# Kernel optimization log

Measured on AMD Instinct MI355X. Metric: run time of the kernel, lower is better.

Reference implementation:

```python
import jax, jax.numpy as jnp
import numpy as np

EPS = 1e-6

def _ln(x, g, b):
    mu = jnp.mean(x, axis=-1, keepdims=True)
    var = jnp.mean(jnp.square(x - mu), axis=-1, keepdims=True)
    return (x - mu) * jax.lax.rsqrt(var + EPS) * g + b

def setup_inputs() -> dict:
    key = jax.random.key(0)
    ks = jax.random.split(key, 8)
    B, T, D = 4, 4096, 1024
    H = 16
    Dff = 4 * D
    s = 1.0 / np.sqrt(D)
    sf = 1.0 / np.sqrt(Dff)
    return {
        "x": jax.random.normal(ks[0], (B, T, D), dtype=jnp.float32),
        "wq": jax.random.uniform(ks[1], (D, D), jnp.float32, -s, s),
        "wk": jax.random.uniform(ks[2], (D, D), jnp.float32, -s, s),
        "wv": jax.random.uniform(ks[3], (D, D), jnp.float32, -s, s),
        "wo": jax.random.uniform(ks[4], (D, D), jnp.float32, -s, s),
        "ln1_g": jnp.ones((D,), jnp.float32),
        "ln1_b": jnp.zeros((D,), jnp.float32),
        "w1": jax.random.uniform(ks[5], (D, Dff), jnp.float32, -s, s),
        "b1": jnp.zeros((Dff,), jnp.float32),
        "w2": jax.random.uniform(ks[6], (Dff, D), jnp.float32, -sf, sf),
        "b2": jnp.zeros((D,), jnp.float32),
        "ln2_g": jnp.ones((D,), jnp.float32),
        "ln2_b": jnp.zeros((D,), jnp.float32),
    }

def reference(x, wq, wk, wv, wo, ln1_g, ln1_b, w1, b1, w2, b2, ln2_g, ln2_b):
    B, T, D = x.shape
    H = 16
    dk = D // H
    x1 = _ln(x, ln1_g, ln1_b)
    q = (x1 @ wq).reshape(B, T, H, dk)
    k = (x1 @ wk).reshape(B, T, H, dk)
    v = (x1 @ wv).reshape(B, T, H, dk)
    # NOTE: faithful to source -- attention mixes HEADS at each token position
    # attn[b,t,h,g] = softmax_g( sum_d q[b,t,h,d]*k[b,t,g,d] / sqrt(dk) )
    attn = jax.nn.softmax(jnp.einsum('bthd,btgd->bthg', q / np.sqrt(dk), k), axis=-1)
    o = jnp.einsum('bthg,btgd->bthd', attn, v)
    # faithful head-major reshape: transpose(1,2).contiguous().view(B,T,-1)
    o = jnp.transpose(o, (0, 2, 1, 3)).reshape(B, T, H * dk)
    o = o @ wo
    q2 = _ln(o + x, ln1_g, ln1_b)  # same layer_norm params reused
    h = jax.nn.gelu(q2 @ w1 + b1, approximate=False)
    y = h @ w2 + b2 + q2
    return _ln(y, ln2_g, ln2_b)
```

## Files before the change

kernel.cpp:

```cpp
#include <hip/hip_runtime.h>


typedef __attribute__((ext_vector_type(8))) short s16x8;
typedef __attribute__((ext_vector_type(4))) short s16x4;
typedef __attribute__((ext_vector_type(4))) float f32x4;

__device__ __forceinline__ short f2bf(float x) {
  unsigned u = __builtin_bit_cast(unsigned, x);
  u = (u + 0x7FFFu + ((u >> 16) & 1u)) >> 16;
  return (short)u;
}
__device__ __forceinline__ float bf2f(short s) {
  unsigned u = ((unsigned)(unsigned short)s) << 16;
  return __builtin_bit_cast(float, u);
}

__device__ __forceinline__ void ld_g2l16(const short* g, const short* l) {
  __builtin_amdgcn_global_load_lds(
      (const __attribute__((address_space(1))) void*)g,
      (__attribute__((address_space(3))) void*)l, 16, 0, 0);
}

__device__ __forceinline__ s16x8 lds_read8(const short* smem, int off) {
  const __attribute__((address_space(3))) short* p =
      (const __attribute__((address_space(3))) short*)smem;
  return *(const __attribute__((address_space(3))) s16x8*)(p + off);
}

__device__ __forceinline__ float fast_gelu(float v) {
  float y = 0.7978845608f * (v + 0.044715f * v * v * v);
  float ay = fabsf(y);
  float t = __expf(-2.0f * ay);
  float th = (1.0f - t) * __frcp_rn(1.0f + t);
  th = (y >= 0.f) ? th : -th;
  return 0.5f * v * (1.0f + th);
}

#define MFMA16(va, vb, vc) \
  __builtin_amdgcn_mfma_f32_16x16x32_bf16(va, vb, vc, 0, 0, 0)

template <int EPI>
__global__ __launch_bounds__(512, 2) void gemm256(
    const short* __restrict__ A, const short* __restrict__ BT,
    void* __restrict__ outp, const float* __restrict__ bias, int N, int K) {
  extern __shared__ __align__(16) short smem[];

  const int t = threadIdx.x;
  const int lane = t & 63, w = t >> 6;
  const int wm = w >> 2, wn = w & 3;

  const int nbn = N >> 8;
  const int oi = (int)blockIdx.x;
  const int seq = oi >> 3;
  const int bq = seq / nbn;
  const int bm = (oi & 7) * 8 + bq;
  const int bn = seq - bq * nbn;

  const int l8 = lane >> 3;
  const int lcw = ((lane & 7) ^ l8) * 8;
  const short* gA = A + (size_t)(bm * 256 + w * 8 + l8) * K + lcw;
  const short* gB = BT + (size_t)(bn * 256 + w * 8 + l8) * K + lcw;
  const int lb = w * 512;

  auto stage = [&](const short* g, int bufo, int h, int kt) {
    const int go = h * 128 * K + kt * 64;
    ld_g2l16(g + go, smem + bufo + h * 8192 + lb);
    ld_g2l16(g + go + 64 * K, smem + bufo + h * 8192 + 4096 + lb);
  };

  const int fr = lane & 15, fc = lane >> 4;
  const int baseA = (wm * 128 + fr) * 64;
  const int baseB = (wn * 64 + fr) * 64;
  const int sl0 = (fc ^ (fr & 7)) * 8;
  const int sl1 = ((4 + fc) ^ (fr & 7)) * 8;

  f32x4 acc[8][4];
#pragma unroll
  for (int m = 0; m < 8; ++m)
#pragma unroll
    for (int n = 0; n < 4; ++n) acc[m][n] = (f32x4){0.f, 0.f, 0.f, 0.f};

  const int nt = K >> 6;

  stage(gA, 0, 0, 0);
  stage(gA, 0, 1, 0);
  stage(gB, 32768, 0, 0);
  stage(gB, 32768, 1, 0);
  if (nt > 1) {
    stage(gA, 16384, 0, 1);
    stage(gA, 16384, 1, 1);
    stage(gB, 49152, 0, 1);
    stage(gB, 49152, 1, 1);
    asm volatile("s_waitcnt vmcnt(8)" ::: "memory");
  } else {
    asm volatile("s_waitcnt vmcnt(0)" ::: "memory");
  }
  __builtin_amdgcn_s_barrier();
  asm volatile("" ::: "memory");

  for (int u = 0; u < nt; ++u) {
    const bool pf = (u + 2 < nt);
    const int pa = (u & 1) << 14;
    const int pb = 32768 + pa;

    s16x8 a0[4][2], a1[4][2], b0[2][2], b1[2][2];
#pragma unroll
    for (int mi = 0; mi < 4; ++mi) {
      a0[mi][0] = lds_read8(smem, pa + baseA + mi * 1024 + sl0);
      a0[mi][1] = lds_read8(smem, pa + baseA + mi * 1024 + sl1);
    }
#pragma unroll
    for (int ni = 0; ni < 2; ++ni) {
      b0[ni][0] = lds_read8(smem, pb + baseB + ni * 1024 + sl0);
      b0[ni][1] = lds_read8(smem, pb + baseB + ni * 1024 + sl1);
    }
#pragma unroll
    for (int ni = 0; ni < 2; ++ni) {
      b1[ni][0] = lds_read8(smem, pb + baseB + 2048 + ni * 1024 + sl0);
      b1[ni][1] = lds_read8(smem, pb + baseB + 2048 + ni * 1024 + sl1);
    }
#pragma unroll
    for (int mi = 0; mi < 4; ++mi) {
      a1[mi][0] = lds_read8(smem, pa + baseA + 4096 + mi * 1024 + sl0);
      a1[mi][1] = lds_read8(smem, pa + baseA + 4096 + mi * 1024 + sl1);
    }

    __builtin_amdgcn_s_setprio(1);
#pragma unroll
    for (int mi = 0; mi < 4; ++mi)
#pragma unroll
      for (int ni = 0; ni < 2; ++ni) {
        acc[mi][ni] = MFMA16(a0[mi][0], b0[ni][0], acc[mi][ni]);
        acc[mi][ni] = MFMA16(a0[mi][1], b0[ni][1], acc[mi][ni]);
      }
#pragma unroll
    for (int mi = 0; mi < 4; ++mi)
#pragma unroll
      for (int ni = 0; ni < 2; ++ni) {
        acc[mi][2 + ni] = MFMA16(a0[mi][0], b1[ni][0], acc[mi][2 + ni]);
        acc[mi][2 + ni] = MFMA16(a0[mi][1], b1[ni][1], acc[mi][2 + ni]);
      }
#pragma unroll
    for (int mi = 0; mi < 4; ++mi)
#pragma unroll
      for (int ni = 0; ni < 2; ++ni) {
        acc[4 + mi][2 + ni] = MFMA16(a1[mi][0], b1[ni][0], acc[4 + mi][2 + ni]);
        acc[4 + mi][2 + ni] = MFMA16(a1[mi][1], b1[ni][1], acc[4 + mi][2 + ni]);
      }
    __builtin_amdgcn_s_setprio(0);

    asm volatile("s_waitcnt lgkmcnt(0)" ::: "memory");
    __builtin_amdgcn_s_barrier();
    asm volatile("" ::: "memory");

    if (pf) {
      stage(gB, pb, 0, u + 2);
      stage(gB, pb, 1, u + 2);
      stage(gA, pa, 0, u + 2);
      stage(gA, pa, 1, u + 2);
    }

    __builtin_amdgcn_s_setprio(1);
#pragma unroll
    for (int mi = 0; mi < 4; ++mi)
#pragma unroll
      for (int ni = 0; ni < 2; ++ni) {
        acc[4 + mi][ni] = MFMA16(a1[mi][0], b0[ni][0], acc[4 + mi][ni]);
        acc[4 + mi][ni] = MFMA16(a1[mi][1], b0[ni][1], acc[4 + mi][ni]);
      }
    __builtin_amdgcn_s_setprio(0);

    if (pf) {
      asm volatile("s_waitcnt vmcnt(8)" ::: "memory");
    } else {
      asm volatile("s_waitcnt vmcnt(0)" ::: "memory");
    }
    __builtin_amdgcn_s_barrier();
    asm volatile("" ::: "memory");
  }

  const int mb = bm * 256 + wm * 128;
  const int nb = bn * 256 + wn * 64;
  const int cr = (lane >> 4) * 4;
  const int cc = lane & 15;
#pragma unroll
  for (int m = 0; m < 8; ++m) {
#pragma unroll
    for (int n = 0; n < 4; ++n) {
#pragma unroll
      for (int r = 0; r < 4; ++r) {
        const size_t row = (size_t)(mb + m * 16 + cr + r);
        const size_t col = (size_t)(nb + n * 16 + cc);
        float v = acc[m][n][r];
        if constexpr (EPI == 0) {
          ((short*)outp)[row * N + col] = f2bf(v);
        } else if constexpr (EPI == 1) {
          ((float*)outp)[row * N + col] = v;
        } else if constexpr (EPI == 2) {
          v += bias[col];
          ((short*)outp)[row * N + col] = f2bf(fast_gelu(v));
        } else {
          float prev = ((float*)outp)[row * N + col];
          v += prev;
          if (bias) v += bias[col];
          ((float*)outp)[row * N + col] = v;
        }
      }
    }
  }
}

template <int EPI>
__global__ __launch_bounds__(512, 4) void gemm128(
    const short* __restrict__ A, const short* __restrict__ BT,
    void* __restrict__ outp, const float* __restrict__ bias, int N, int K) {
  extern __shared__ __align__(16) short smem[];

  const int t = threadIdx.x;
  const int lane = t & 63, w = t >> 6;
  const int wm = w >> 2, wn = w & 3;

  const int nbn = N >> 8;
  const int oi = (int)blockIdx.x;
  const int seq = oi >> 3;
  const int bq = seq / nbn;
  const int bm = (oi & 7) * 16 + bq;
  const int bn = seq - bq * nbn;

  const int lr = lane >> 2;
  const int lc = ((lane & 3) - ((lane >> 3) & 3)) & 3;
  const short* gA = A + (size_t)(bm * 128 + lr) * K + lc * 8;
  const short* gB = BT + (size_t)(bn * 256 + lr) * K + lc * 8;

  auto stageT = [&](int par, int kt) {
    ld_g2l16(gA + (size_t)(w * 16) * K + kt * 32, smem + par + w * 512);
    ld_g2l16(gB + (size_t)(2 * w * 16) * K + kt * 32,
             smem + par + 4096 + 2 * w * 512);
    ld_g2l16(gB + (size_t)((2 * w + 1) * 16) * K + kt * 32,
             smem + par + 4096 + (2 * w + 1) * 512);
  };

  const int fr = lane & 15, fc = lane >> 4;
  const int sl = ((fc + (fr >> 1)) & 3) * 8;
  const int baseA = (wm * 64 + fr) * 32 + sl;
  const int baseB = 4096 + (wn * 64 + fr) * 32 + sl;

  f32x4 acc[4][4];
#pragma unroll
  for (int m = 0; m < 4; ++m)
#pragma unroll
    for (int n = 0; n < 4; ++n) acc[m][n] = (f32x4){0.f, 0.f, 0.f, 0.f};

  const int nt = K >> 5;

  stageT(0, 0);
  stageT(12288, 1);
  asm volatile("s_waitcnt vmcnt(3)" ::: "memory");
  __builtin_amdgcn_s_barrier();
  asm volatile("" ::: "memory");

  int pcur = 0, pnxt = 12288, pprv = 24576;
  for (int u = 0; u < nt; ++u) {
    const bool pf = (u + 2 < nt);

    if (pf) stageT(pprv, u + 2);

    s16x8 a[4], b[4];
#pragma unroll
    for (int i = 0; i < 4; ++i)
      a[i] = lds_read8(smem, pcur + baseA + i * 512);
#pragma unroll
    for (int i = 0; i < 4; ++i)
      b[i] = lds_read8(smem, pcur + baseB + i * 512);

    __builtin_amdgcn_s_setprio(1);
#pragma unroll
    for (int mi = 0; mi < 4; ++mi)
#pragma unroll
      for (int ni = 0; ni < 4; ++ni)
        acc[mi][ni] = MFMA16(a[mi], b[ni], acc[mi][ni]);
    __builtin_amdgcn_s_setprio(0);

    asm volatile("s_waitcnt lgkmcnt(0)" ::: "memory");
    if (pf) {
      asm volatile("s_waitcnt vmcnt(3)" ::: "memory");
    } else {
      asm volatile("s_waitcnt vmcnt(0)" ::: "memory");
    }
    __builtin_amdgcn_s_barrier();
    asm volatile("" ::: "memory");

    const int tmp = pcur;
    pcur = pnxt;
    pnxt = pprv;
    pprv = tmp;
  }

  const int mb = bm * 128 + wm * 64;
  const int nb = bn * 256 + wn * 64;
  const int cr = (lane >> 4) * 4;
  const int cc = lane & 15;
#pragma unroll
  for (int m = 0; m < 4; ++m) {
#pragma unroll
    for (int n = 0; n < 4; ++n) {
#pragma unroll
      for (int r = 0; r < 4; ++r) {
        const size_t row = (size_t)(mb + m * 16 + cr + r);
        const size_t col = (size_t)(nb + n * 16 + cc);
        float v = acc[m][n][r];
        if constexpr (EPI == 0) {
          ((short*)outp)[row * N + col] = f2bf(v);
        } else if constexpr (EPI == 1) {
          ((float*)outp)[row * N + col] = v;
        } else if constexpr (EPI == 2) {
          v += bias[col];
          ((short*)outp)[row * N + col] = f2bf(fast_gelu(v));
        } else {
          float prev = ((float*)outp)[row * N + col];
          v += prev;
          if (bias) v += bias[col];
          ((float*)outp)[row * N + col] = v;
        }
      }
    }
  }
}

__global__ __launch_bounds__(256) void ln_k(
    const float* __restrict__ in, const float* __restrict__ add,
    const float* __restrict__ g, const float* __restrict__ b,
    float* __restrict__ outf, short* __restrict__ outb) {
  const int row = blockIdx.x;
  const size_t off = (size_t)row * 1024;
  const int t = threadIdx.x;
  float4 v = ((const float4*)(in + off))[t];
  if (add) {
    float4 w = ((const float4*)(add + off))[t];
    v.x += w.x; v.y += w.y; v.z += w.z; v.w += w.w;
  }
  float s = v.x + v.y + v.z + v.w;
  float ss = v.x * v.x + v.y * v.y + v.z * v.z + v.w * v.w;
#pragma unroll
  for (int o = 32; o > 0; o >>= 1) {
    s += __shfl_xor(s, o, 64);
    ss += __shfl_xor(ss, o, 64);
  }
  __shared__ float ps[4], pss[4];
  const int lane = t & 63, wave = t >> 6;
  if (lane == 0) { ps[wave] = s; pss[wave] = ss; }
  __syncthreads();
  s = ps[0] + ps[1] + ps[2] + ps[3];
  ss = pss[0] + pss[1] + pss[2] + pss[3];
  const float mean = s * (1.0f / 1024.0f);
  const float var = ss * (1.0f / 1024.0f) - mean * mean;
  const float rstd = rsqrtf(var + 1e-6f);
  const float4 gv = ((const float4*)g)[t];
  const float4 bv = ((const float4*)b)[t];
  float4 o4;
  o4.x = (v.x - mean) * rstd * gv.x + bv.x;
  o4.y = (v.y - mean) * rstd * gv.y + bv.y;
  o4.z = (v.z - mean) * rstd * gv.z + bv.z;
  o4.w = (v.w - mean) * rstd * gv.w + bv.w;
  if (outf) ((float4*)(outf + off))[t] = o4;
  if (outb) {
    s16x4 ob;
    ob[0] = f2bf(o4.x); ob[1] = f2bf(o4.y);
    ob[2] = f2bf(o4.z); ob[3] = f2bf(o4.w);
    *(s16x4*)(outb + off + t * 4) = ob;
  }
}

__device__ __forceinline__ void wconv_tile(const float* __restrict__ W,
                                           short* __restrict__ WT, int K,
                                           int N, int n0, int k0,
                                           float (*tile)[33], int c, int r) {
#pragma unroll
  for (int rr = r; rr < 32; rr += 8)
    tile[rr][c] = W[(size_t)(k0 + rr) * N + n0 + c];
  __syncthreads();
#pragma unroll
  for (int rr = r; rr < 32; rr += 8)
    WT[(size_t)(n0 + rr) * K + k0 + c] = f2bf(tile[c][rr]);
}

__global__ __launch_bounds__(256) void wconv_all(
    const float* __restrict__ wq, const float* __restrict__ wk,
    const float* __restrict__ wv, const float* __restrict__ wo,
    const float* __restrict__ w1, const float* __restrict__ w2,
    short* __restrict__ WQKVT, short* __restrict__ WOT,
    short* __restrict__ W1T, short* __restrict__ W2aT,
    short* __restrict__ W2bT) {
  __shared__ float tile[32][33];
  const int t = threadIdx.x;
  const int c = t & 31, r = t >> 5;
  const int i = blockIdx.x;
  if (i < 4096) {
    const int seg = i >> 10, j = i & 1023;
    const int n0 = (j & 31) * 32, k0 = (j >> 5) * 32;
    const float* src = (seg == 0) ? wq : (seg == 1) ? wk : (seg == 2) ? wv : wo;
    short* dst = (seg == 3) ? WOT : WQKVT + (size_t)seg * 1024 * 1024;
    wconv_tile(src, dst, 1024, 1024, n0, k0, tile, c, r);
  } else if (i < 8192) {
    const int j = i - 4096;
    const int n0 = (j & 127) * 32, k0 = (j >> 7) * 32;
    wconv_tile(w1, W1T, 1024, 4096, n0, k0, tile, c, r);
  } else if (i < 10240) {
    const int j = i - 8192;
    const int n0 = (j & 31) * 32, k0 = (j >> 5) * 32;
    wconv_tile(w2, W2aT, 2048, 1024, n0, k0, tile, c, r);
  } else {
    const int j = i - 10240;
    const int n0 = (j & 31) * 32, k0 = (j >> 5) * 32;
    wconv_tile(w2 + (size_t)2048 * 1024, W2bT, 2048, 1024, n0, k0, tile, c, r);
  }
}

__global__ __launch_bounds__(256) void attn_k(const short* __restrict__ qkv,
                                              short* __restrict__ omix) {
  __shared__ float Qs[4][16][65];
  __shared__ float Ks[4][16][65];
  __shared__ float Vs[4][16][65];
  __shared__ float Ps[4][16][17];
  const int lane = threadIdx.x & 63;
  const int wave = threadIdx.x >> 6;
  const int tok = blockIdx.x * 4 + wave;
  const short* base = qkv + (size_t)tok * 3072;

#pragma unroll
  for (int half = 0; half < 2; half++) {
    const int e = half * 512 + lane * 8;
    const int h = e >> 6, d = e & 63;
    s16x8 rq = *(const s16x8*)(base + e);
    s16x8 rk = *(const s16x8*)(base + 1024 + e);
    s16x8 rv = *(const s16x8*)(base + 2048 + e);
#pragma unroll
    for (int j = 0; j < 8; j++) {
      Qs[wave][h][d + j] = bf2f(rq[j]);
      Ks[wave][h][d + j] = bf2f(rk[j]);
      Vs[wave][h][d + j] = bf2f(rv[j]);
    }
  }
  __syncthreads();

  const int h = lane & 15;
  const int g0 = (lane >> 4) * 4;
  float sc[4] = {0.f, 0.f, 0.f, 0.f};
  for (int d = 0; d < 64; d++) {
    const float qv = Qs[wave][h][d];
#pragma unroll
    for (int i = 0; i < 4; i++) sc[i] += qv * Ks[wave][g0 + i][d];
  }
#pragma unroll
  for (int i = 0; i < 4; i++) sc[i] *= 0.125f;
  float m = fmaxf(fmaxf(sc[0], sc[1]), fmaxf(sc[2], sc[3]));
  m = fmaxf(m, __shfl_xor(m, 16, 64));
  m = fmaxf(m, __shfl_xor(m, 32, 64));
  float e[4], sum = 0.f;
#pragma unroll
  for (int i = 0; i < 4; i++) { e[i] = __expf(sc[i] - m); sum += e[i]; }
  sum += __shfl_xor(sum, 16, 64);
  sum += __shfl_xor(sum, 32, 64);
  const float inv = __frcp_rn(sum);
#pragma unroll
  for (int i = 0; i < 4; i++) Ps[wave][h][g0 + i] = e[i] * inv;
  __syncthreads();

  const int d0 = (lane >> 4) * 16;
  float o[16];
#pragma unroll
  for (int dd = 0; dd < 16; dd++) o[dd] = 0.f;
  for (int gg = 0; gg < 16; gg++) {
    const float pv = Ps[wave][h][gg];
#pragma unroll
    for (int dd = 0; dd < 16; dd++) o[dd] += pv * Vs[wave][gg][d0 + dd];
  }

  const int b = tok >> 12, t = tok & 4095;
  const size_t dst =
      ((size_t)(b * 4096 + h * 256 + (t >> 4))) * 1024 + (t & 15) * 64 + d0;
  s16x8 w0, w1;
#pragma unroll
  for (int j = 0; j < 8; j++) { w0[j] = f2bf(o[j]); w1[j] = f2bf(o[8 + j]); }
  *(s16x8*)(omix + dst) = w0;
  *(s16x8*)(omix + dst + 8) = w1;
}

extern "C" void kernel_launch(void* const* d_in, const int* in_sizes, int n_in,
                              void* d_out, int out_size, void* d_ws,
                              size_t ws_size, hipStream_t stream) {
  const float* x    = (const float*)d_in[0];
  const float* wq   = (const float*)d_in[1];
  const float* wk   = (const float*)d_in[2];
  const float* wv   = (const float*)d_in[3];
  const float* wo   = (const float*)d_in[4];
  const float* ln1g = (const float*)d_in[5];
  const float* ln1b = (const float*)d_in[6];
  const float* w1   = (const float*)d_in[7];
  const float* b1   = (const float*)d_in[8];
  const float* w2   = (const float*)d_in[9];
  const float* b2   = (const float*)d_in[10];
  const float* ln2g = (const float*)d_in[11];
  const float* ln2b = (const float*)d_in[12];
  float* out = (float*)d_out;

  char* ws = (char*)d_ws;
  const size_t MB = 1024ull * 1024ull;
  const size_t NEEDED = 152 * MB;
  if (ws_size < NEEDED) return;

  short* QKV  = (short*)(ws + 0);
  short* Q2B  = (short*)(ws + 0);
  short* Hbuf = (short*)(ws + 32 * MB);
  short* X1 = (short*)(ws + 96 * MB);
  short* WQKVT = (short*)(ws + 128 * MB);
  short* WOT   = (short*)(ws + 134 * MB);
  short* W1T   = (short*)(ws + 136 * MB);
  short* W2aT  = (short*)(ws + 144 * MB);
  short* W2bT  = (short*)(ws + 148 * MB);

  const dim3 B256(256);
  const dim3 B512(512);
  const unsigned LDS256 = 131072;
  const unsigned LDS128 = 73728;

  static bool attr_done = false;
  if (!attr_done) {
    attr_done = true;
    void (*k0)(const short*, const short*, void*, const float*, int, int) =
        gemm256<0>;
    (void)hipFuncSetAttribute((const void*)k0,
        hipFuncAttributeMaxDynamicSharedMemorySize, (int)LDS256);
    void (*h1)(const short*, const short*, void*, const float*, int, int) =
        gemm128<1>;
    void (*h2)(const short*, const short*, void*, const float*, int, int) =
        gemm128<2>;
    void (*h4)(const short*, const short*, void*, const float*, int, int) =
        gemm128<4>;
    (void)hipFuncSetAttribute((const void*)h1,
        hipFuncAttributeMaxDynamicSharedMemorySize, (int)LDS128);
    (void)hipFuncSetAttribute((const void*)h2,
        hipFuncAttributeMaxDynamicSharedMemorySize, (int)LDS128);
    (void)hipFuncSetAttribute((const void*)h4,
        hipFuncAttributeMaxDynamicSharedMemorySize, (int)LDS128);
  }

  wconv_all<<<dim3(12288), B256, 0, stream>>>(wq, wk, wv, wo, w1, w2, WQKVT,
                                              WOT, W1T, W2aT, W2bT);

  ln_k<<<16384, B256, 0, stream>>>(x, nullptr, ln1g, ln1b, nullptr, X1);

  gemm256<0><<<dim3(768), B512, LDS256, stream>>>(X1, WQKVT, QKV, nullptr,
                                                  3072, 1024);

  attn_k<<<4096, B256, 0, stream>>>(QKV, X1);

  gemm128<1><<<dim3(512), B512, LDS128, stream>>>(X1, WOT, out, nullptr,
                                                  1024, 1024);

  ln_k<<<16384, B256, 0, stream>>>(out, x, ln1g, ln1b, out, Q2B);

  gemm128<2><<<dim3(1024), B512, LDS128, stream>>>(Q2B, W1T, Hbuf, b1,
                                                   2048, 1024);
  gemm128<4><<<dim3(512), B512, LDS128, stream>>>(Hbuf, W2aT, out, nullptr,
                                                  1024, 2048);

  gemm128<2><<<dim3(1024), B512, LDS128, stream>>>(Q2B, W1T + 2048 * 1024,
                                                   Hbuf, b1 + 2048, 2048,
                                                   1024);
  gemm128<4><<<dim3(512), B512, LDS128, stream>>>(Hbuf, W2bT, out, b2,
                                                  1024, 2048);

  ln_k<<<16384, B256, 0, stream>>>(out, nullptr, ln2g, ln2b, out, nullptr);
}
```

Before: 776.9 us.

## Restructure 256x256 GEMM into fine-grained staged pipeline and use it everywhere

Rewrites the 256x256 GEMM main loop to process two K-tiles per iteration, splitting each into four MFMA quadrants. Global-to-LDS loads for the next tile are issued in half-tile pieces between those quadrants, with a barrier between each piece. The 128-row GEMM variant is removed, and the output projection and both MLP GEMMs now launch the 256 tile kernel with half as many blocks. The aim is to overlap loads with MFMA work more evenly and to raise data reuse. The cost is many more barriers per iteration, and fewer blocks (256 or 512 on a large-CU device) may leave occupancy or wave balance worse.

```diff
diff --git a/kernel.cpp b/kernel.cpp
--- a/kernel.cpp
+++ b/kernel.cpp
@@ -39,6 +39,11 @@
 #define MFMA16(va, vb, vc) \
   __builtin_amdgcn_mfma_f32_16x16x32_bf16(va, vb, vc, 0, 0, 0)
 
+#define BARRIER() do { __builtin_amdgcn_s_barrier(); \
+                       asm volatile("" ::: "memory"); } while (0)
+#define LGKM0() asm volatile("s_waitcnt lgkmcnt(0)" ::: "memory")
+#define VMC(n) asm volatile("s_waitcnt vmcnt(" #n ")" ::: "memory")
+
 template <int EPI>
 __global__ __launch_bounds__(512, 2) void gemm256(
     const short* __restrict__ A, const short* __restrict__ BT,
@@ -62,7 +67,7 @@
   const short* gB = BT + (size_t)(bn * 256 + w * 8 + l8) * K + lcw;
   const int lb = w * 512;
 
-  auto stage = [&](const short* g, int bufo, int h, int kt) {
+  auto stageH = [&](const short* g, int bufo, int h, int kt) {
     const int go = h * 128 * K + kt * 64;
     ld_g2l16(g + go, smem + bufo + h * 8192 + lb);
     ld_g2l16(g + go + 64 * K, smem + bufo + h * 8192 + 4096 + lb);
@@ -80,51 +85,36 @@
 #pragma unroll
     for (int n = 0; n < 4; ++n) acc[m][n] = (f32x4){0.f, 0.f, 0.f, 0.f};
 
+  s16x8 a0[4][2], a1[4][2], b0[2][2], b1[2][2];
+
   const int nt = K >> 6;
 
-  stage(gA, 0, 0, 0);
-  stage(gA, 0, 1, 0);
-  stage(gB, 32768, 0, 0);
-  stage(gB, 32768, 1, 0);
-  if (nt > 1) {
-    stage(gA, 16384, 0, 1);
-    stage(gA, 16384, 1, 1);
-    stage(gB, 49152, 0, 1);
-    stage(gB, 49152, 1, 1);
-    asm volatile("s_waitcnt vmcnt(8)" ::: "memory");
-  } else {
-    asm volatile("s_waitcnt vmcnt(0)" ::: "memory");
-  }
-  __builtin_amdgcn_s_barrier();
-  asm volatile("" ::: "memory");
-
-  for (int u = 0; u < nt; ++u) {
-    const bool pf = (u + 2 < nt);
-    const int pa = (u & 1) << 14;
-    const int pb = 32768 + pa;
-
-    s16x8 a0[4][2], a1[4][2], b0[2][2], b1[2][2];
+  stageH(gA, 0, 0, 0);
+  stageH(gA, 0, 1, 0);
+  stageH(gB, 32768, 0, 0);
+  stageH(gB, 32768, 1, 0);
+  stageH(gA, 16384, 0, 1);
+  stageH(gA, 16384, 1, 1);
+  VMC(4);
+  BARRIER();
+
+  for (int it = 0; it < (nt >> 1); ++it) {
+    const int u = it << 1;
+    const bool more = (u + 2 < nt);
+
 #pragma unroll
     for (int mi = 0; mi < 4; ++mi) {
-      a0[mi][0] = lds_read8(smem, pa + baseA + mi * 1024 + sl0);
-      a0[mi][1] = lds_read8(smem, pa + baseA + mi * 1024 + sl1);
+      a0[mi][0] = lds_read8(smem, baseA + mi * 1024 + sl0);
+      a0[mi][1] = lds_read8(smem, baseA + mi * 1024 + sl1);
     }
 #pragma unroll
     for (int ni = 0; ni < 2; ++ni) {
-      b0[ni][0] = lds_read8(smem, pb + baseB + ni * 1024 + sl0);
-      b0[ni][1] = lds_read8(smem, pb + baseB + ni * 1024 + sl1);
-    }
-#pragma unroll
-    for (int ni = 0; ni < 2; ++ni) {
-      b1[ni][0] = lds_read8(smem, pb + baseB + 2048 + ni * 1024 + sl0);
-      b1[ni][1] = lds_read8(smem, pb + baseB + 2048 + ni * 1024 + sl1);
-    }
-#pragma unroll
-    for (int mi = 0; mi < 4; ++mi) {
-      a1[mi][0] = lds_read8(smem, pa + baseA + 4096 + mi * 1024 + sl0);
-      a1[mi][1] = lds_read8(smem, pa + baseA + 4096 + mi * 1024 + sl1);
-    }
-
+      b0[ni][0] = lds_read8(smem, 32768 + baseB + ni * 1024 + sl0);
+      b0[ni][1] = lds_read8(smem, 32768 + baseB + ni * 1024 + sl1);
+    }
+    stageH(gB, 49152, 0, u + 1);
+    BARRIER();
+    LGKM0();
     __builtin_amdgcn_s_setprio(1);
 #pragma unroll
     for (int mi = 0; mi < 4; ++mi)
@@ -133,6 +123,50 @@
         acc[mi][ni] = MFMA16(a0[mi][0], b0[ni][0], acc[mi][ni]);
         acc[mi][ni] = MFMA16(a0[mi][1], b0[ni][1], acc[mi][ni]);
       }
+    __builtin_amdgcn_s_setprio(0);
+    BARRIER();
+
+#pragma unroll
+    for (int mi = 0; mi < 4; ++mi) {
+      a1[mi][0] = lds_read8(smem, baseA + 4096 + mi * 1024 + sl0);
+      a1[mi][1] = lds_read8(smem, baseA + 4096 + mi * 1024 + sl1);
+    }
+    stageH(gB, 49152, 1, u + 1);
+    BARRIER();
+    LGKM0();
+    __builtin_amdgcn_s_setprio(1);
+#pragma unroll
+    for (int mi = 0; mi < 4; ++mi)
+#pragma unroll
+      for (int ni = 0; ni < 2; ++ni) {
+        acc[4 + mi][ni] = MFMA16(a1[mi][0], b0[ni][0], acc[4 + mi][ni]);
+        acc[4 + mi][ni] = MFMA16(a1[mi][1], b0[ni][1], acc[4 + mi][ni]);
+      }
+    __builtin_amdgcn_s_setprio(0);
+    BARRIER();
+
+#pragma unroll
+    for (int ni = 0; ni < 2; ++ni) {
+      b1[ni][0] = lds_read8(smem, 32768 + baseB + 2048 + ni * 1024 + sl0);
+      b1[ni][1] = lds_read8(smem, 32768 + baseB + 2048 + ni * 1024 + sl1);
+    }
+    if (more) stageH(gA, 0, 0, u + 2);
+    BARRIER();
+    LGKM0();
+    __builtin_amdgcn_s_setprio(1);
+#pragma unroll
+    for (int mi = 0; mi < 4; ++mi)
+#pragma unroll
+      for (int ni = 0; ni < 2; ++ni) {
+        acc[4 + mi][2 + ni] = MFMA16(a1[mi][0], b1[ni][0], acc[4 + mi][2 + ni]);
+        acc[4 + mi][2 + ni] = MFMA16(a1[mi][1], b1[ni][1], acc[4 + mi][2 + ni]);
+      }
+    __builtin_amdgcn_s_setprio(0);
+    BARRIER();
+
+    if (more) stageH(gA, 0, 1, u + 2);
+    BARRIER();
+    __builtin_amdgcn_s_setprio(1);
 #pragma unroll
     for (int mi = 0; mi < 4; ++mi)
 #pragma unroll
@@ -140,6 +174,66 @@
         acc[mi][2 + ni] = MFMA16(a0[mi][0], b1[ni][0], acc[mi][2 + ni]);
         acc[mi][2 + ni] = MFMA16(a0[mi][1], b1[ni][1], acc[mi][2 + ni]);
       }
+    __builtin_amdgcn_s_setprio(0);
+    if (more) {
+      VMC(4);
+    } else {
+      VMC(0);
+    }
+    BARRIER();
+
+#pragma unroll
+    for (int mi = 0; mi < 4; ++mi) {
+      a0[mi][0] = lds_read8(smem, 16384 + baseA + mi * 1024 + sl0);
+      a0[mi][1] = lds_read8(smem, 16384 + baseA + mi * 1024 + sl1);
+    }
+#pragma unroll
+    for (int ni = 0; ni < 2; ++ni) {
+      b0[ni][0] = lds_read8(smem, 49152 + baseB + ni * 1024 + sl0);
+      b0[ni][1] = lds_read8(smem, 49152 + baseB + ni * 1024 + sl1);
+    }
+    if (more) stageH(gB, 32768, 0, u + 2);
+    BARRIER();
+    LGKM0();
+    __builtin_amdgcn_s_setprio(1);
+#pragma unroll
+    for (int mi = 0; mi < 4; ++mi)
+#pragma unroll
+      for (int ni = 0; ni < 2; ++ni) {
+        acc[mi][ni] = MFMA16(a0[mi][0], b0[ni][0], acc[mi][ni]);
+        acc[mi][ni] = MFMA16(a0[mi][1], b0[ni][1], acc[mi][ni]);
+      }
+    __builtin_amdgcn_s_setprio(0);
+    BARRIER();
+
+#pragma unroll
+    for (int mi = 0; mi < 4; ++mi) {
+      a1[mi][0] = lds_read8(smem, 16384 + baseA + 4096 + mi * 1024 + sl0);
+      a1[mi][1] = lds_read8(smem, 16384 + baseA + 4096 + mi * 1024 + sl1);
+    }
+    if (more) stageH(gB, 32768, 1, u + 2);
+    BARRIER();
+    LGKM0();
+    __builtin_amdgcn_s_setprio(1);
+#pragma unroll
+    for (int mi = 0; mi < 4; ++mi)
+#pragma unroll
+      for (int ni = 0; ni < 2; ++ni) {
+        acc[4 + mi][ni] = MFMA16(a1[mi][0], b0[ni][0], acc[4 + mi][ni]);
+        acc[4 + mi][ni] = MFMA16(a1[mi][1], b0[ni][1], acc[4 + mi][ni]);
+      }
+    __builtin_amdgcn_s_setprio(0);
+    BARRIER();
+
+#pragma unroll
+    for (int ni = 0; ni < 2; ++ni) {
+      b1[ni][0] = lds_read8(smem, 49152 + baseB + 2048 + ni * 1024 + sl0);
+      b1[ni][1] = lds_read8(smem, 49152 + baseB + 2048 + ni * 1024 + sl1);
+    }
+    if (more) stageH(gA, 16384, 0, u + 3);
+    BARRIER();
+    LGKM0();
+    __builtin_amdgcn_s_setprio(1);
 #pragma unroll
     for (int mi = 0; mi < 4; ++mi)
 #pragma unroll
@@ -148,35 +242,25 @@
         acc[4 + mi][2 + ni] = MFMA16(a1[mi][1], b1[ni][1], acc[4 + mi][2 + ni]);
       }
     __builtin_amdgcn_s_setprio(0);
-
-    asm volatile("s_waitcnt lgkmcnt(0)" ::: "memory");
-    __builtin_amdgcn_s_barrier();
-    asm volatile("" ::: "memory");
-
-    if (pf) {
-      stage(gB, pb, 0, u + 2);
-      stage(gB, pb, 1, u + 2);
-      stage(gA, pa, 0, u + 2);
-      stage(gA, pa, 1, u + 2);
-    }
-
-    __builtin_amdgcn_s_setprio(1);
-#pragma unroll
-    for (int mi = 0; mi < 4; ++mi)
-#pragma unroll
-      for (int ni = 0; ni < 2; ++ni) {
-        acc[4 + mi][ni] = MFMA16(a1[mi][0], b0[ni][0], acc[4 + mi][ni]);
-        acc[4 + mi][ni] = MFMA16(a1[mi][1], b0[ni][1], acc[4 + mi][ni]);
-      }
-    __builtin_amdgcn_s_setprio(0);
-
-    if (pf) {
-      asm volatile("s_waitcnt vmcnt(8)" ::: "memory");
+    BARRIER();
+
+    if (more) stageH(gA, 16384, 1, u + 3);
+    BARRIER();
+    __builtin_amdgcn_s_setprio(1);
+#pragma unroll
+    for (int mi = 0; mi < 4; ++mi)
+#pragma unroll
+      for (int ni = 0; ni < 2; ++ni) {
+        acc[mi][2 + ni] = MFMA16(a0[mi][0], b1[ni][0], acc[mi][2 + ni]);
+        acc[mi][2 + ni] = MFMA16(a0[mi][1], b1[ni][1], acc[mi][2 + ni]);
+      }
+    __builtin_amdgcn_s_setprio(0);
+    if (more) {
+      VMC(4);
     } else {
-      asm volatile("s_waitcnt vmcnt(0)" ::: "memory");
-    }
-    __builtin_amdgcn_s_barrier();
-    asm volatile("" ::: "memory");
+      VMC(0);
+    }
+    BARRIER();
   }
 
   const int mb = bm * 256 + wm * 128;
@@ -185,123 +269,6 @@
   const int cc = lane & 15;
 #pragma unroll
   for (int m = 0; m < 8; ++m) {
-#pragma unroll
-    for (int n = 0; n < 4; ++n) {
-#pragma unroll
-      for (int r = 0; r < 4; ++r) {
-        const size_t row = (size_t)(mb + m * 16 + cr + r);
-        const size_t col = (size_t)(nb + n * 16 + cc);
-        float v = acc[m][n][r];
-        if constexpr (EPI == 0) {
-          ((short*)outp)[row * N + col] = f2bf(v);
-        } else if constexpr (EPI == 1) {
-          ((float*)outp)[row * N + col] = v;
-        } else if constexpr (EPI == 2) {
-          v += bias[col];
-          ((short*)outp)[row * N + col] = f2bf(fast_gelu(v));
-        } else {
-          float prev = ((float*)outp)[row * N + col];
-          v += prev;
-          if (bias) v += bias[col];
-          ((float*)outp)[row * N + col] = v;
-        }
-      }
-    }
-  }
-}
-
-template <int EPI>
-__global__ __launch_bounds__(512, 4) void gemm128(
-    const short* __restrict__ A, const short* __restrict__ BT,
-    void* __restrict__ outp, const float* __restrict__ bias, int N, int K) {
-  extern __shared__ __align__(16) short smem[];
-
-  const int t = threadIdx.x;
-  const int lane = t & 63, w = t >> 6;
-  const int wm = w >> 2, wn = w & 3;
-
-  const int nbn = N >> 8;
-  const int oi = (int)blockIdx.x;
-  const int seq = oi >> 3;
-  const int bq = seq / nbn;
-  const int bm = (oi & 7) * 16 + bq;
-  const int bn = seq - bq * nbn;
-
-  const int lr = lane >> 2;
-  const int lc = ((lane & 3) - ((lane >> 3) & 3)) & 3;
-  const short* gA = A + (size_t)(bm * 128 + lr) * K + lc * 8;
-  const short* gB = BT + (size_t)(bn * 256 + lr) * K + lc * 8;
-
-  auto stageT = [&](int par, int kt) {
-    ld_g2l16(gA + (size_t)(w * 16) * K + kt * 32, smem + par + w * 512);
-    ld_g2l16(gB + (size_t)(2 * w * 16) * K + kt * 32,
-             smem + par + 4096 + 2 * w * 512);
-    ld_g2l16(gB + (size_t)((2 * w + 1) * 16) * K + kt * 32,
-             smem + par + 4096 + (2 * w + 1) * 512);
-  };
-
-  const int fr = lane & 15, fc = lane >> 4;
-  const int sl = ((fc + (fr >> 1)) & 3) * 8;
-  const int baseA = (wm * 64 + fr) * 32 + sl;
-  const int baseB = 4096 + (wn * 64 + fr) * 32 + sl;
-
-  f32x4 acc[4][4];
-#pragma unroll
-  for (int m = 0; m < 4; ++m)
-#pragma unroll
-    for (int n = 0; n < 4; ++n) acc[m][n] = (f32x4){0.f, 0.f, 0.f, 0.f};
-
-  const int nt = K >> 5;
-
-  stageT(0, 0);
-  stageT(12288, 1);
-  asm volatile("s_waitcnt vmcnt(3)" ::: "memory");
-  __builtin_amdgcn_s_barrier();
-  asm volatile("" ::: "memory");
-
-  int pcur = 0, pnxt = 12288, pprv = 24576;
-  for (int u = 0; u < nt; ++u) {
-    const bool pf = (u + 2 < nt);
-
-    if (pf) stageT(pprv, u + 2);
-
-    s16x8 a[4], b[4];
-#pragma unroll
-    for (int i = 0; i < 4; ++i)
-      a[i] = lds_read8(smem, pcur + baseA + i * 512);
-#pragma unroll
-    for (int i = 0; i < 4; ++i)
-      b[i] = lds_read8(smem, pcur + baseB + i * 512);
-
-    __builtin_amdgcn_s_setprio(1);
-#pragma unroll
-    for (int mi = 0; mi < 4; ++mi)
-#pragma unroll
-      for (int ni = 0; ni < 4; ++ni)
-        acc[mi][ni] = MFMA16(a[mi], b[ni], acc[mi][ni]);
-    __builtin_amdgcn_s_setprio(0);
-
-    asm volatile("s_waitcnt lgkmcnt(0)" ::: "memory");
-    if (pf) {
-      asm volatile("s_waitcnt vmcnt(3)" ::: "memory");
-    } else {
-      asm volatile("s_waitcnt vmcnt(0)" ::: "memory");
-    }
-    __builtin_amdgcn_s_barrier();
-    asm volatile("" ::: "memory");
-
-    const int tmp = pcur;
-    pcur = pnxt;
-    pnxt = pprv;
-    pprv = tmp;
-  }
-
-  const int mb = bm * 128 + wm * 64;
-  const int nb = bn * 256 + wn * 64;
-  const int cr = (lane >> 4) * 4;
-  const int cc = lane & 15;
-#pragma unroll
-  for (int m = 0; m < 4; ++m) {
 #pragma unroll
     for (int n = 0; n < 4; ++n) {
 #pragma unroll
@@ -522,27 +489,26 @@
   const dim3 B256(256);
   const dim3 B512(512);
   const unsigned LDS256 = 131072;
-  const unsigned LDS128 = 73728;
 
   static bool attr_done = false;
   if (!attr_done) {
     attr_done = true;
     void (*k0)(const short*, const short*, void*, const float*, int, int) =
         gemm256<0>;
+    void (*k1)(const short*, const short*, void*, const float*, int, int) =
+        gemm256<1>;
+    void (*k2)(const short*, const short*, void*, const float*, int, int) =
+        gemm256<2>;
+    void (*k4)(const short*, const short*, void*, const float*, int, int) =
+        gemm256<4>;
     (void)hipFuncSetAttribute((const void*)k0,
         hipFuncAttributeMaxDynamicSharedMemorySize, (int)LDS256);
-    void (*h1)(const short*, const short*, void*, const float*, int, int) =
-        gemm128<1>;
-    void (*h2)(const short*, const short*, void*, const float*, int, int) =
-        gemm128<2>;
-    void (*h4)(const short*, const short*, void*, const float*, int, int) =
-        gemm128<4>;
-    (void)hipFuncSetAttribute((const void*)h1,
-        hipFuncAttributeMaxDynamicSharedMemorySize, (int)LDS128);
-    (void)hipFuncSetAttribute((const void*)h2,
-        hipFuncAttributeMaxDynamicSharedMemorySize, (int)LDS128);
-    (void)hipFuncSetAttribute((const void*)h4,
-        hipFuncAttributeMaxDynamicSharedMemorySize, (int)LDS128);
+    (void)hipFuncSetAttribute((const void*)k1,
+        hipFuncAttributeMaxDynamicSharedMemorySize, (int)LDS256);
+    (void)hipFuncSetAttribute((const void*)k2,
+        hipFuncAttributeMaxDynamicSharedMemorySize, (int)LDS256);
+    (void)hipFuncSetAttribute((const void*)k4,
+        hipFuncAttributeMaxDynamicSharedMemorySize, (int)LDS256);
   }
 
   wconv_all<<<dim3(12288), B256, 0, stream>>>(wq, wk, wv, wo, w1, w2, WQKVT,
@@ -555,20 +521,20 @@
 
   attn_k<<<4096, B256, 0, stream>>>(QKV, X1);
 
-  gemm128<1><<<dim3(512), B512, LDS128, stream>>>(X1, WOT, out, nullptr,
+  gemm256<1><<<dim3(256), B512, LDS256, stream>>>(X1, WOT, out, nullptr,
                                                   1024, 1024);
 
   ln_k<<<16384, B256, 0, stream>>>(out, x, ln1g, ln1b, out, Q2B);
 
-  gemm128<2><<<dim3(1024), B512, LDS128, stream>>>(Q2B, W1T, Hbuf, b1,
-                                                   2048, 1024);
-  gemm128<4><<<dim3(512), B512, LDS128, stream>>>(Hbuf, W2aT, out, nullptr,
+  gemm256<2><<<dim3(512), B512, LDS256, stream>>>(Q2B, W1T, Hbuf, b1,
+                                                  2048, 1024);
+  gemm256<4><<<dim3(256), B512, LDS256, stream>>>(Hbuf, W2aT, out, nullptr,
                                                   1024, 2048);
 
-  gemm128<2><<<dim3(1024), B512, LDS128, stream>>>(Q2B, W1T + 2048 * 1024,
-                                                   Hbuf, b1 + 2048, 2048,
-                                                   1024);
-  gemm128<4><<<dim3(512), B512, LDS128, stream>>>(Hbuf, W2bT, out, b2,
+  gemm256<2><<<dim3(512), B512, LDS256, stream>>>(Q2B, W1T + 2048 * 1024,
+                                                  Hbuf, b1 + 2048, 2048,
+                                                  1024);
+  gemm256<4><<<dim3(256), B512, LDS256, stream>>>(Hbuf, W2bT, out, b2,
                                                   1024, 2048);
 
   ln_k<<<16384, B256, 0, stream>>>(out, nullptr, ln2g, ln2b, out, nullptr);
```

New measurement: 874.3 us. 1.13x slower.
